# Optimization experiments

Measured on AMD Instinct MI355X. Metric: run time of the kernel, lower is better.

## Reference

```python
import jax, jax.numpy as jnp
import numpy as np

I, H, L, O = 128, 512, 2, 1  # input_size, hidden_size, num_layers, output_size
B, S = 64, 512


def setup_inputs() -> dict:
    key = jax.random.key(0)
    ks = jax.random.split(key, 12)
    inp = {
        "x": jax.random.normal(ks[0], (B, S, I), dtype=jnp.float32),
        "theta": jax.random.normal(ks[1], (I, H), dtype=jnp.float32) * 0.02,
        "phi": jax.random.normal(ks[2], (I, H), dtype=jnp.float32) * 0.02,
        "theta_noise": jax.random.normal(ks[3], (I, H), dtype=jnp.float32) * 0.01,
        "phi_noise": jax.random.normal(ks[4], (I, H), dtype=jnp.float32) * 0.01,
        # stacked per-layer LSTM weights (all layers take H-dim input)
        "W_ih": jax.random.normal(ks[5], (L, 4 * H, H), dtype=jnp.float32) * (1.0 / np.sqrt(H)),
        "W_hh": jax.random.normal(ks[6], (L, 4 * H, H), dtype=jnp.float32) * (1.0 / np.sqrt(H)),
        "b_ih": jax.random.normal(ks[7], (L, 4 * H), dtype=jnp.float32) * (1.0 / np.sqrt(H)),
        "b_hh": jax.random.normal(ks[8], (L, 4 * H), dtype=jnp.float32) * (1.0 / np.sqrt(H)),
        "fc1_w": jax.random.normal(ks[9], (H, H), dtype=jnp.float32) * (1.0 / np.sqrt(H)),
        "fc1_b": jnp.zeros((H,), dtype=jnp.float32),
        "fc2_w": jax.random.normal(ks[10], (O, H), dtype=jnp.float32) * (1.0 / np.sqrt(H)),
        "fc2_b": jnp.zeros((O,), dtype=jnp.float32),
    }
    return inp


def _lstm_layer(xs, Wih, Whh, bih, bhh):
    # xs: (S, B, H) -> hs: (S, B, H). PyTorch gate order: i, f, g, o.
    Bn = xs.shape[1]
    Hn = Whh.shape[1]
    # precompute input projections for all timesteps in one GEMM
    x_proj = jnp.einsum("sbh,gh->sbg", xs, Wih) + bih + bhh  # (S, B, 4H)

    def step(carry, xp):
        h, c = carry
        gates = xp + h @ Whh.T  # (B, 4H)
        i, f, g, o = jnp.split(gates, 4, axis=-1)
        i = jax.nn.sigmoid(i)
        f = jax.nn.sigmoid(f)
        g = jnp.tanh(g)
        o = jax.nn.sigmoid(o)
        c = f * c + i * g
        h = o * jnp.tanh(c)
        return (h, c), h

    h0 = jnp.zeros((Bn, Hn), dtype=xs.dtype)
    c0 = jnp.zeros((Bn, Hn), dtype=xs.dtype)
    _, hs = jax.lax.scan(step, (h0, c0), x_proj)
    return hs


def reference(x, theta, phi, theta_noise, phi_noise, W_ih, W_hh, b_ih, b_hh,
              fc1_w, fc1_b, fc2_w, fc2_b):
    # QuantumInspiredLayer: |x @ (cos(theta+n) + i*sin(phi+n))| done as two real GEMMs
    real = jnp.einsum("bsi,ih->bsh", x, jnp.cos(theta + theta_noise))
    imag = jnp.einsum("bsi,ih->bsh", x, jnp.sin(phi + phi_noise))
    q = jnp.sqrt(real * real + imag * imag)  # (B, S, H)

    hs = jnp.transpose(q, (1, 0, 2))  # (S, B, H)
    n_layers = W_ih.shape[0]
    for l in range(n_layers):
        hs = _lstm_layer(hs, W_ih[l], W_hh[l], b_ih[l], b_hh[l])
    last = hs[-1]  # (B, H) -- out[:, -1, :]

    h1 = jax.nn.relu(last @ fc1_w.T + fc1_b)
    # dropout is identity in eval mode
    return h1 @ fc2_w.T + fc2_b  # (B, O)
```

## Files before the change

kernel.cpp:

```cpp
#include <hip/hip_runtime.h>


typedef _Float16 f16;
typedef _Float16 f16x8 __attribute__((ext_vector_type(8)));
typedef float f32x4 __attribute__((ext_vector_type(4)));
typedef unsigned long long u64;

#define MFMA16(a, b, c) __builtin_amdgcn_mfma_f32_16x16x32_f16((a), (b), (c), 0, 0, 0)
#define LD_AG(p) __hip_atomic_load((p), __ATOMIC_RELAXED, __HIP_MEMORY_SCOPE_AGENT)
#define ST_AG(p, v) __hip_atomic_store((p), (v), __ATOMIC_RELAXED, __HIP_MEMORY_SCOPE_AGENT)

#define OFF_Q16 0UL
#define OFF_X16 33554432UL
#define OFF_W16 41943040UL
#define OFF_COS 50331648UL
#define OFF_SIN 50462720UL
#define OFF_BSUM 50593792UL
#define OFF_HBUF 50610176UL
#define OFF_HLAST 51003392UL
#define OFF_FC1WT 51134464UL
#define OFF_FLG 52183040UL
#define WS_NEEDED 52215808UL

__global__ __launch_bounds__(256) void k_prep(
    const float* __restrict__ x, const float* __restrict__ theta,
    const float* __restrict__ phi, const float* __restrict__ thn,
    const float* __restrict__ phn, const float* __restrict__ Wih,
    const float* __restrict__ Whh, const float* __restrict__ bih,
    const float* __restrict__ bhh, const float* __restrict__ fc1w,
    f16* __restrict__ x16, f16* __restrict__ w16, f16* __restrict__ cosT,
    f16* __restrict__ sinT, float* __restrict__ bsum, float* __restrict__ fc1wT,
    f16* __restrict__ hbuf, unsigned* __restrict__ flg) {
  const int T1 = 4194304;
  const int T2 = T1 + 4194304;
  const int T3 = T2 + 65536;
  const int T4 = T3 + 262144;
  const int T5 = T4 + 4096;
  const int T6 = T5 + 196608;
  const int T7 = T6 + 8192;
  for (int idx = blockIdx.x * 256 + threadIdx.x; idx < T7; idx += gridDim.x * 256) {
    if (idx < T1) {
      int s = idx >> 13, rem = idx & 8191, b = rem >> 7, i = rem & 127;
      x16[idx] = (f16)x[b * 65536 + s * 128 + i];
    } else if (idx < T2) {
      int j = idx - T1;
      int l = j >> 21, rem = j & 2097151, r = rem >> 10, k = rem & 1023;
      float v = (k < 512) ? Wih[((size_t)l * 2048 + r) * 512 + k]
                          : Whh[((size_t)l * 2048 + r) * 512 + (k - 512)];
      w16[(size_t)l * 2097152 + (size_t)r * 1024 + k] = (f16)v;
    } else if (idx < T3) {
      int e = idx - T2;
      int i = e >> 9, h = e & 511;
      cosT[h * 128 + i] = (f16)cosf(theta[e] + thn[e]);
      sinT[h * 128 + i] = (f16)sinf(phi[e] + phn[e]);
    } else if (idx < T4) {
      int e = idx - T3;
      int n = e >> 9, k = e & 511;
      fc1wT[k * 512 + n] = fc1w[e];
    } else if (idx < T5) {
      int e = idx - T4;
      bsum[e] = bih[e] + bhh[e];
    } else if (idx < T6) {
      hbuf[idx - T5] = (f16)0.f;
    } else {
      flg[idx - T6] = 0u;
    }
  }
}

__global__ __launch_bounds__(256) void k_quantum(
    const f16* __restrict__ x16, const f16* __restrict__ cosT,
    const f16* __restrict__ sinT, f16* __restrict__ q16) {
  __shared__ __align__(16) f16 a_lds[64 * 136];
  const int tid = threadIdx.x;
  const int r0 = blockIdx.x * 64, h0 = blockIdx.y * 128;
#pragma unroll
  for (int g = 0; g < 4; ++g) {
    int G = g * 256 + tid, row = G >> 4, col = G & 15;
    *(uint4*)((char*)a_lds + row * 272 + col * 16) =
        *(const uint4*)(x16 + (size_t)(r0 + row) * 128 + col * 8);
  }
  __syncthreads();
  const int wv = tid >> 6, lane = tid & 63, n15 = lane & 15, quad = lane >> 4;
  const int nb = h0 + wv * 32;
  f32x4 ac[4][2], as_[4][2];
#pragma unroll
  for (int mt = 0; mt < 4; ++mt)
#pragma unroll
    for (int nt = 0; nt < 2; ++nt) {
      ac[mt][nt] = (f32x4){0.f, 0.f, 0.f, 0.f};
      as_[mt][nt] = (f32x4){0.f, 0.f, 0.f, 0.f};
    }
#pragma unroll
  for (int it = 0; it < 4; ++it) {
    f16x8 a[4];
#pragma unroll
    for (int mt = 0; mt < 4; ++mt)
      a[mt] = *(const f16x8*)((const char*)a_lds + (mt * 16 + n15) * 272 + it * 64 + quad * 16);
#pragma unroll
    for (int nt = 0; nt < 2; ++nt) {
      const f16x8 bc = *(const f16x8*)(cosT + (size_t)(nb + nt * 16 + n15) * 128 + it * 32 + quad * 8);
      const f16x8 bs = *(const f16x8*)(sinT + (size_t)(nb + nt * 16 + n15) * 128 + it * 32 + quad * 8);
#pragma unroll
      for (int mt = 0; mt < 4; ++mt) {
        ac[mt][nt] = MFMA16(a[mt], bc, ac[mt][nt]);
        as_[mt][nt] = MFMA16(a[mt], bs, as_[mt][nt]);
      }
    }
  }
#pragma unroll
  for (int mt = 0; mt < 4; ++mt)
#pragma unroll
    for (int nt = 0; nt < 2; ++nt)
#pragma unroll
      for (int r = 0; r < 4; ++r) {
        int row = r0 + mt * 16 + quad * 4 + r;
        int col = nb + nt * 16 + n15;
        float re = ac[mt][nt][r], im = as_[mt][nt][r];
        q16[(size_t)row * 512 + col] = (f16)sqrtf(re * re + im * im);
      }
}

__device__ __forceinline__ f16x8 lds_a(const char* astage, int row, int it, int quad) {
  int pos = (it * 4 + quad) ^ (row & 7);
  return *(const f16x8*)(astage + row * 2048 + pos * 16);
}
__device__ __forceinline__ float sigf(float x) { return 1.f / (1.f + __expf(-x)); }
__device__ __forceinline__ float tanhf_fast(float x) { return 1.f - 2.f / (__expf(2.f * x) + 1.f); }

__global__ __launch_bounds__(512, 2) void k_rec(
    const f16* __restrict__ q16, const f16* __restrict__ w16,
    const float* __restrict__ bsum, f16* __restrict__ h0buf,
    f16* __restrict__ h1buf, float* __restrict__ hlast, unsigned* flg) {
  __shared__ __align__(16) char astage[32768];
  __shared__ float gbuf[16 * 132];

  const int tid = threadIdx.x, lane = tid & 63, wv = tid >> 6;
  const int n15 = lane & 15, quad = lane >> 4;
  const int qg = wv >> 1, ch = wv & 1;
  const int dom = blockIdx.x >> 5, role = blockIdx.x & 31;
  const int l = role >> 4, c0 = (role & 15) * 32;
  const int b0 = dom * 16;

  f16x8 wf[32];
  {
    const f16* wbase = w16 + ((size_t)l * 2048 + (size_t)(qg * 512 + c0 + ch * 16 + n15)) * 1024 + quad * 8;
#pragma unroll
    for (int it = 0; it < 32; ++it) wf[it] = *(const f16x8*)(wbase + it * 32);
  }
  float bb[4][2];
#pragma unroll
  for (int g = 0; g < 4; ++g)
#pragma unroll
    for (int j = 0; j < 2; ++j)
      bb[g][j] = bsum[l * 2048 + g * 512 + c0 + (tid & 15) * 2 + j];
  float cs0 = 0.f, cs1 = 0.f;

  unsigned* f0 = flg + (size_t)(dom * 2 + 0) * 1024;
  unsigned* f1 = flg + (size_t)(dom * 2 + 1) * 1024;
  unsigned* myflag = (l ? f1 : f0) + (size_t)(role & 15) * 64;
  const int pl = lane & 31;
  const unsigned* pollp = (pl < 16) ? (f0 + pl * 64) : (f1 + (pl - 16) * 64);

  const int srow = tid >> 5, scg = tid & 31;
  const int g0 = scg * 2;
  char* a_x0 = astage + srow * 2048 + ((g0 ^ (srow & 7)) * 16);
  char* a_x1 = astage + srow * 2048 + (((g0 + 1) ^ (srow & 7)) * 16);
  char* a_h0 = a_x0 + 1024;
  char* a_h1 = a_x1 + 1024;
  const size_t soff = (size_t)srow * 512 + scg * 16;
  const size_t h0base = (size_t)dom * 4 * 8192;
  const size_t h1base = (size_t)dom * 2 * 8192;

  for (int t = 0; t <= 511; ++t) {
    if (l == 0) {
      const f16* src = q16 + ((size_t)(t * 64 + b0 + srow)) * 512 + scg * 16;
      uint4 v0 = *(const uint4*)src;
      uint4 v1 = *(const uint4*)(src + 8);
      *(uint4*)a_x0 = v0;
      *(uint4*)a_x1 = v1;
    }
    if (t >= 1 || l == 1) {
      const int mytgt = (l == 0) ? ((pl < 16) ? t : (t - 2))
                                 : ((pl < 16) ? (t + 1) : t);
      while (true) {
        int f = (int)LD_AG(pollp);
        if (__all(f >= mytgt)) break;
        __builtin_amdgcn_s_sleep(1);
      }
    }
    if (l == 0) {
      const u64* hs0 = (const u64*)(h0buf + h0base + (size_t)((t - 1) & 3) * 8192 + soff);
      u64 x0 = LD_AG(hs0);
      u64 x1 = LD_AG(hs0 + 1);
      u64 x2 = LD_AG(hs0 + 2);
      u64 x3 = LD_AG(hs0 + 3);
      ((u64*)a_h0)[0] = x0; ((u64*)a_h0)[1] = x1;
      ((u64*)a_h1)[0] = x2; ((u64*)a_h1)[1] = x3;
    } else {
      const u64* hs0 = (const u64*)(h0buf + h0base + (size_t)(t & 3) * 8192 + soff);
      u64 x0 = LD_AG(hs0);
      u64 x1 = LD_AG(hs0 + 1);
      u64 x2 = LD_AG(hs0 + 2);
      u64 x3 = LD_AG(hs0 + 3);
      const u64* hs1 = (const u64*)(h1buf + h1base + (size_t)((t - 1) & 1) * 8192 + soff);
      u64 y0 = LD_AG(hs1);
      u64 y1 = LD_AG(hs1 + 1);
      u64 y2 = LD_AG(hs1 + 2);
      u64 y3 = LD_AG(hs1 + 3);
      ((u64*)a_x0)[0] = x0; ((u64*)a_x0)[1] = x1;
      ((u64*)a_x1)[0] = x2; ((u64*)a_x1)[1] = x3;
      ((u64*)a_h0)[0] = y0; ((u64*)a_h0)[1] = y1;
      ((u64*)a_h1)[0] = y2; ((u64*)a_h1)[1] = y3;
    }
    __syncthreads();

    f32x4 acc = (f32x4){0.f, 0.f, 0.f, 0.f};
#pragma unroll
    for (int it = 0; it < 32; ++it)
      acc = MFMA16(lds_a(astage, n15, it, quad), wf[it], acc);
#pragma unroll
    for (int r = 0; r < 4; ++r)
      gbuf[(quad * 4 + r) * 132 + qg * 33 + ch * 16 + n15] = acc[r];
    __syncthreads();

    if (tid < 256) {
      const int b = tid >> 4, jc = (tid & 15) * 2;
      float hv[2];
#pragma unroll
      for (int j = 0; j < 2; ++j) {
        const float* gb = gbuf + b * 132 + jc + j;
        float gi = gb[0] + bb[0][j];
        float gf = gb[33] + bb[1][j];
        float gg = gb[66] + bb[2][j];
        float go = gb[99] + bb[3][j];
        float cprev = j ? cs1 : cs0;
        float c = sigf(gf) * cprev + sigf(gi) * tanhf_fast(gg);
        if (j) cs1 = c; else cs0 = c;
        hv[j] = sigf(go) * tanhf_fast(c);
      }
      union { f16 h2[2]; unsigned u; } pk;
      pk.h2[0] = (f16)hv[0];
      pk.h2[1] = (f16)hv[1];
      f16* dst = (l == 0)
          ? h0buf + h0base + (size_t)(t & 3) * 8192 + (size_t)b * 512 + c0 + jc
          : h1buf + h1base + (size_t)(t & 1) * 8192 + (size_t)b * 512 + c0 + jc;
      ST_AG((unsigned*)dst, pk.u);
      if (l == 1 && t == 511) {
        hlast[(size_t)(b0 + b) * 512 + c0 + jc] = hv[0];
        hlast[(size_t)(b0 + b) * 512 + c0 + jc + 1] = hv[1];
      }
    }
    __syncthreads();
    if (tid == 0) ST_AG(myflag, (unsigned)(t + 1));
  }
}

__global__ __launch_bounds__(512) void k_fc(
    const float* __restrict__ hlast, const float* __restrict__ fc1wT,
    const float* __restrict__ fc1b, const float* __restrict__ fc2w,
    const float* __restrict__ fc2b, float* __restrict__ out) {
  __shared__ float hrow[512];
  __shared__ float red[8];
  const int b = blockIdx.x, tid = threadIdx.x;
  hrow[tid] = hlast[b * 512 + tid];
  __syncthreads();
  float acc = 0.f;
#pragma unroll 8
  for (int k = 0; k < 512; ++k) acc += hrow[k] * fc1wT[k * 512 + tid];
  float h1 = acc + fc1b[tid];
  h1 = h1 > 0.f ? h1 : 0.f;
  float v = h1 * fc2w[tid];
#pragma unroll
  for (int off = 32; off >= 1; off >>= 1) v += __shfl_down(v, off);
  if ((tid & 63) == 0) red[tid >> 6] = v;
  __syncthreads();
  if (tid == 0) {
    float s = 0.f;
#pragma unroll
    for (int w = 0; w < 8; ++w) s += red[w];
    out[b] = s + fc2b[0];
  }
}

extern "C" void kernel_launch(void* const* d_in, const int* in_sizes, int n_in,
                              void* d_out, int out_size, void* d_ws, size_t ws_size,
                              hipStream_t stream) {
  if (ws_size < WS_NEEDED) return;

  const float* x = (const float*)d_in[0];
  const float* theta = (const float*)d_in[1];
  const float* phi = (const float*)d_in[2];
  const float* thn = (const float*)d_in[3];
  const float* phn = (const float*)d_in[4];
  const float* Wih = (const float*)d_in[5];
  const float* Whh = (const float*)d_in[6];
  const float* bih = (const float*)d_in[7];
  const float* bhh = (const float*)d_in[8];
  const float* fc1w = (const float*)d_in[9];
  const float* fc1b = (const float*)d_in[10];
  const float* fc2w = (const float*)d_in[11];
  const float* fc2b = (const float*)d_in[12];

  char* ws = (char*)d_ws;
  f16* q16 = (f16*)(ws + OFF_Q16);
  f16* x16 = (f16*)(ws + OFF_X16);
  f16* w16 = (f16*)(ws + OFF_W16);
  f16* cosT = (f16*)(ws + OFF_COS);
  f16* sinT = (f16*)(ws + OFF_SIN);
  float* bsum = (float*)(ws + OFF_BSUM);
  f16* h0buf = (f16*)(ws + OFF_HBUF);
  f16* h1buf = h0buf + 131072;
  float* hlast = (float*)(ws + OFF_HLAST);
  float* fc1wT = (float*)(ws + OFF_FC1WT);
  unsigned* flg = (unsigned*)(ws + OFF_FLG);

  k_prep<<<2048, 256, 0, stream>>>(x, theta, phi, thn, phn, Wih, Whh, bih, bhh, fc1w,
                                   x16, w16, cosT, sinT, bsum, fc1wT, h0buf, flg);
  k_quantum<<<dim3(512, 4, 1), 256, 0, stream>>>(x16, cosT, sinT, q16);
  k_rec<<<128, 512, 0, stream>>>(q16, w16, bsum, h0buf, h1buf, hlast, flg);
  k_fc<<<64, 512, 0, stream>>>(hlast, fc1wT, fc1b, fc2w, fc2b, (float*)d_out);
}
```

Baseline: 1.853 ms.

## Store full layer-0 hidden history to decouple layer-0 from layer-1 waits

Layer-0 hidden states now go to a buffer holding all 513 timesteps per domain instead of a 4-slot ring. Layer-0 therefore no longer polls layer-1 flags for slot reuse and can run ahead, removing the cross-layer back-pressure wait. The sleep in the poll loops is dropped, and the MFMA chain is split into two independent accumulators to shorten the dependency chain. The cost is a larger workspace, more global writes, and busier polling.

```diff
diff --git a/kernel.cpp b/kernel.cpp
--- a/kernel.cpp
+++ b/kernel.cpp
@@ -16,11 +16,12 @@
 #define OFF_COS 50331648UL
 #define OFF_SIN 50462720UL
 #define OFF_BSUM 50593792UL
-#define OFF_HBUF 50610176UL
-#define OFF_HLAST 51003392UL
-#define OFF_FC1WT 51134464UL
-#define OFF_FLG 52183040UL
-#define WS_NEEDED 52215808UL
+#define OFF_H1 50610176UL
+#define OFF_HLAST 50741248UL
+#define OFF_FC1WT 50872320UL
+#define OFF_FLG 51920896UL
+#define OFF_H0 51953664UL
+#define WS_NEEDED 85573632UL
 
 __global__ __launch_bounds__(256) void k_prep(
     const float* __restrict__ x, const float* __restrict__ theta,
@@ -30,13 +31,13 @@
     const float* __restrict__ bhh, const float* __restrict__ fc1w,
     f16* __restrict__ x16, f16* __restrict__ w16, f16* __restrict__ cosT,
     f16* __restrict__ sinT, float* __restrict__ bsum, float* __restrict__ fc1wT,
-    f16* __restrict__ hbuf, unsigned* __restrict__ flg) {
+    f16* __restrict__ h0buf, f16* __restrict__ h1buf, unsigned* __restrict__ flg) {
   const int T1 = 4194304;
   const int T2 = T1 + 4194304;
   const int T3 = T2 + 65536;
   const int T4 = T3 + 262144;
   const int T5 = T4 + 4096;
-  const int T6 = T5 + 196608;
+  const int T6 = T5 + 98304;
   const int T7 = T6 + 8192;
   for (int idx = blockIdx.x * 256 + threadIdx.x; idx < T7; idx += gridDim.x * 256) {
     if (idx < T1) {
@@ -61,7 +62,14 @@
       int e = idx - T4;
       bsum[e] = bih[e] + bhh[e];
     } else if (idx < T6) {
-      hbuf[idx - T5] = (f16)0.f;
+      int e = idx - T5;
+      if (e < 65536) {
+        h1buf[e] = (f16)0.f;
+      } else {
+        int e2 = e - 65536;
+        int dm = e2 >> 13, o = e2 & 8191;
+        h0buf[(size_t)dm * 513 * 8192 + o] = (f16)0.f;
+      }
     } else {
       flg[idx - T6] = 0u;
     }
@@ -159,8 +167,10 @@
   unsigned* f0 = flg + (size_t)(dom * 2 + 0) * 1024;
   unsigned* f1 = flg + (size_t)(dom * 2 + 1) * 1024;
   unsigned* myflag = (l ? f1 : f0) + (size_t)(role & 15) * 64;
-  const int pl = lane & 31;
-  const unsigned* pollp = (pl < 16) ? (f0 + pl * 64) : (f1 + (pl - 16) * 64);
+  const unsigned* pollp;
+  if (l == 0) pollp = f0 + (size_t)(lane & 15) * 64;
+  else pollp = (lane < 32) ? (f0 + (size_t)(lane & 15) * 64)
+                           : (f1 + (size_t)(lane & 15) * 64);
 
   const int srow = tid >> 5, scg = tid & 31;
   const int g0 = scg * 2;
@@ -169,7 +179,7 @@
   char* a_h0 = a_x0 + 1024;
   char* a_h1 = a_x1 + 1024;
   const size_t soff = (size_t)srow * 512 + scg * 16;
-  const size_t h0base = (size_t)dom * 4 * 8192;
+  const size_t h0base = (size_t)dom * 513 * 8192;
   const size_t h1base = (size_t)dom * 2 * 8192;
 
   for (int t = 0; t <= 511; ++t) {
@@ -180,17 +190,22 @@
       *(uint4*)a_x0 = v0;
       *(uint4*)a_x1 = v1;
     }
-    if (t >= 1 || l == 1) {
-      const int mytgt = (l == 0) ? ((pl < 16) ? t : (t - 2))
-                                 : ((pl < 16) ? (t + 1) : t);
+    if (l == 0) {
+      if (t >= 1) {
+        while (true) {
+          int f = (int)LD_AG(pollp);
+          if (__all(f >= t)) break;
+        }
+      }
+    } else {
+      const int mytgt = (lane < 32) ? (t + 1) : t;
       while (true) {
         int f = (int)LD_AG(pollp);
         if (__all(f >= mytgt)) break;
-        __builtin_amdgcn_s_sleep(1);
       }
     }
     if (l == 0) {
-      const u64* hs0 = (const u64*)(h0buf + h0base + (size_t)((t - 1) & 3) * 8192 + soff);
+      const u64* hs0 = (const u64*)(h0buf + h0base + (size_t)t * 8192 + soff);
       u64 x0 = LD_AG(hs0);
       u64 x1 = LD_AG(hs0 + 1);
       u64 x2 = LD_AG(hs0 + 2);
@@ -198,7 +213,7 @@
       ((u64*)a_h0)[0] = x0; ((u64*)a_h0)[1] = x1;
       ((u64*)a_h1)[0] = x2; ((u64*)a_h1)[1] = x3;
     } else {
-      const u64* hs0 = (const u64*)(h0buf + h0base + (size_t)(t & 3) * 8192 + soff);
+      const u64* hs0 = (const u64*)(h0buf + h0base + (size_t)(t + 1) * 8192 + soff);
       u64 x0 = LD_AG(hs0);
       u64 x1 = LD_AG(hs0 + 1);
       u64 x2 = LD_AG(hs0 + 2);
@@ -215,13 +230,16 @@
     }
     __syncthreads();
 
-    f32x4 acc = (f32x4){0.f, 0.f, 0.f, 0.f};
-#pragma unroll
-    for (int it = 0; it < 32; ++it)
-      acc = MFMA16(lds_a(astage, n15, it, quad), wf[it], acc);
+    f32x4 acca = (f32x4){0.f, 0.f, 0.f, 0.f};
+    f32x4 accb = (f32x4){0.f, 0.f, 0.f, 0.f};
+#pragma unroll
+    for (int it = 0; it < 16; ++it) {
+      acca = MFMA16(lds_a(astage, n15, 2 * it, quad), wf[2 * it], acca);
+      accb = MFMA16(lds_a(astage, n15, 2 * it + 1, quad), wf[2 * it + 1], accb);
+    }
 #pragma unroll
     for (int r = 0; r < 4; ++r)
-      gbuf[(quad * 4 + r) * 132 + qg * 33 + ch * 16 + n15] = acc[r];
+      gbuf[(quad * 4 + r) * 132 + qg * 33 + ch * 16 + n15] = acca[r] + accb[r];
     __syncthreads();
 
     if (tid < 256) {
@@ -243,7 +261,7 @@
       pk.h2[0] = (f16)hv[0];
       pk.h2[1] = (f16)hv[1];
       f16* dst = (l == 0)
-          ? h0buf + h0base + (size_t)(t & 3) * 8192 + (size_t)b * 512 + c0 + jc
+          ? h0buf + h0base + (size_t)(t + 1) * 8192 + (size_t)b * 512 + c0 + jc
           : h1buf + h1base + (size_t)(t & 1) * 8192 + (size_t)b * 512 + c0 + jc;
       ST_AG((unsigned*)dst, pk.u);
       if (l == 1 && t == 511) {
@@ -309,14 +327,14 @@
   f16* cosT = (f16*)(ws + OFF_COS);
   f16* sinT = (f16*)(ws + OFF_SIN);
   float* bsum = (float*)(ws + OFF_BSUM);
-  f16* h0buf = (f16*)(ws + OFF_HBUF);
-  f16* h1buf = h0buf + 131072;
+  f16* h1buf = (f16*)(ws + OFF_H1);
+  f16* h0buf = (f16*)(ws + OFF_H0);
   float* hlast = (float*)(ws + OFF_HLAST);
   float* fc1wT = (float*)(ws + OFF_FC1WT);
   unsigned* flg = (unsigned*)(ws + OFF_FLG);
 
   k_prep<<<2048, 256, 0, stream>>>(x, theta, phi, thn, phn, Wih, Whh, bih, bhh, fc1w,
-                                   x16, w16, cosT, sinT, bsum, fc1wT, h0buf, flg);
+                                   x16, w16, cosT, sinT, bsum, fc1wT, h0buf, h1buf, flg);
   k_quantum<<<dim3(512, 4, 1), 256, 0, stream>>>(x16, cosT, sinT, q16);
   k_rec<<<128, 512, 0, stream>>>(q16, w16, bsum, h0buf, h1buf, hlast, flg);
   k_fc<<<64, 512, 0, stream>>>(hlast, fc1wT, fc1b, fc2w, fc2b, (float*)d_out);
```

Measured after the change: 1.936 ms. 4.4% more time.
